# Optimization experiments

Measured on AMD Instinct MI355X. Metric: run time of the kernel, lower is better.

The kernel has to match this reference:

```python
import jax, jax.numpy as jnp
import numpy as np

N, F, E, B, D = 100000, 256, 128, 10000, 32
GAMMA, ZETA = -0.1, 1.1  # hard-concrete stretch params of L0Dense


def setup_inputs() -> dict:
    key = jax.random.key(0)
    ks = jax.random.split(key, 12)
    return {
        "nodes": jax.random.randint(ks[0], (B,), 0, N),
        "neigh_idx": jax.random.randint(ks[1], (B, D), 0, N),
        "neigh_mask": jax.random.bernoulli(ks[2], 0.9, (B, D)),
        "feature": jax.random.normal(ks[3], (N, F), jnp.float32),
        "W": jax.random.normal(ks[4], (F, E), jnp.float32) * 0.05,
        "b": jnp.zeros((E,), jnp.float32),
        "qz_loga": jax.random.normal(ks[5], (F,), jnp.float32),
        "att1_w": jax.random.normal(ks[6], (2 * E, E), jnp.float32) * 0.05,
        "att1_b": jnp.zeros((E,), jnp.float32),
        "att2_w": jax.random.normal(ks[7], (E, E), jnp.float32) * 0.05,
        "att2_b": jnp.zeros((E,), jnp.float32),
        "att3_w": jax.random.normal(ks[8], (E, 1), jnp.float32) * 0.05,
        "att3_b": jnp.zeros((1,), jnp.float32),
    }


def reference(nodes, neigh_idx, neigh_mask, feature, W, b, qz_loga,
              att1_w, att1_b, att2_w, att2_b, att3_w, att3_b):
    # L0Dense, deterministic (eval) hard-concrete gate on input dims
    z = jnp.clip(jax.nn.sigmoid(qz_loga) * (ZETA - GAMMA) + GAMMA, 0.0, 1.0)
    We = W * z[:, None]                                  # [F, E]

    node_feat = feature[nodes] @ We + b                   # [B, E]
    neigh_feat = feature[neigh_idx] @ We + b              # [B, D, E]

    # GraphRec-style attention MLP over (neighbor, center) pairs
    h = jnp.concatenate(
        [neigh_feat, jnp.broadcast_to(node_feat[:, None, :], neigh_feat.shape)],
        axis=-1)                                          # [B, D, 2E]
    h = jax.nn.relu(h @ att1_w + att1_b)
    h = jax.nn.relu(h @ att2_w + att2_b)
    scores = (h @ att3_w + att3_b)[..., 0]                # [B, D]
    scores = jnp.where(neigh_mask, scores, -1e30)
    att = jax.nn.softmax(scores, axis=-1)                 # [B, D]

    agg = jnp.einsum('bd,bde->be', att, neigh_feat)       # weighted sum
    has_neigh = neigh_mask.any(axis=-1, keepdims=True)
    return jnp.where(has_neigh, agg, node_feat)           # n==0 fallback
```

## Files before the change

kernel.cpp:

```cpp
#include <hip/hip_runtime.h>
#include <hip/hip_bf16.h>
#include <math.h>

#define NN 100000
#define FF 256
#define EE 128
#define BB_ 10000
#define DD 32

typedef __attribute__((ext_vector_type(8))) short short8;
typedef __attribute__((ext_vector_type(4))) float f32x4;

__device__ __forceinline__ short f2bf(float f) {
  __hip_bfloat16 h = __float2bfloat16(f);
  union { __hip_bfloat16 h; short s; } u; u.h = h;
  return u.s;
}
__device__ __forceinline__ float bf2f(short s) {
  union { unsigned u; float f; } v;
  v.u = ((unsigned)(unsigned short)s) << 16;
  return v.f;
}

__global__ __launch_bounds__(256) void k_prep(
    const float* __restrict__ W, const float* __restrict__ qz,
    const float* __restrict__ a1w, const float* __restrict__ a2w,
    const float* __restrict__ bb,
    float* __restrict__ Wef32, short* __restrict__ BT2,
    short* __restrict__ a1wTc, short* __restrict__ w2T,
    float* __restrict__ bias2) {
  int i = blockIdx.x * 256 + threadIdx.x;
  if (i < 32768) {
    int f = i >> 7, e = i & 127;
    float g = qz[f];
    float s = 1.0f / (1.0f + expf(-g));
    float z = fminf(fmaxf(s * 1.2f - 0.1f, 0.0f), 1.0f);
    float v = W[f * 128 + e] * z;
    Wef32[f * 128 + e] = v;
    BT2[e * 256 + f] = f2bf(v);
  } else if (i < 49152) {
    int t = i - 32768; int n = t >> 7, k = t & 127;
    a1wTc[n * 128 + k] = f2bf(a1w[(128 + k) * 128 + n]);
  } else if (i < 65536) {
    int t = i - 49152; int n = t >> 7, k = t & 127;
    w2T[n * 128 + k] = f2bf(a2w[k * 128 + n]);
  } else if (i < 65664) {
    bias2[i - 65536] = bb[i - 65536];
  }
}

__global__ __launch_bounds__(256) void k_compose(
    const float* __restrict__ Wef32, const float* __restrict__ a1w,
    const float* __restrict__ a1b, const float* __restrict__ bb,
    short* __restrict__ BT2, float* __restrict__ bias2) {
  const int n = blockIdx.x;
  const int f = threadIdx.x;
  float s = 0.f;
  for (int e = 0; e < 128; ++e)
    s = fmaf(a1w[e * 128 + n], Wef32[f * 128 + e], s);
  BT2[(size_t)(128 + n) * 256 + f] = f2bf(s);
  if (f == 0) {
    float by = a1b[n];
    for (int e = 0; e < 128; ++e) by = fmaf(bb[e], a1w[e * 128 + n], by);
    bias2[128 + n] = by;
  }
}

template <int K, int LDA, int LDC, bool AF32, bool OUTBF16>
__global__ __launch_bounds__(256) void k_mm(
    const void* __restrict__ Ap, const short* __restrict__ BT,
    const float* __restrict__ bias, const int* __restrict__ idx,
    void* __restrict__ Cp, int M) {
  __shared__ short As[128 * 64];
  __shared__ short Bs[128 * 64];
  const int tid = threadIdx.x;
  const int mb = blockIdx.x * 128;
  const int col0 = blockIdx.y * 128;
  const int wave = tid >> 6, lane = tid & 63;
  const int wr = wave >> 1, wc = wave & 1;
  const int l15 = lane & 15, lg = lane >> 4;

  size_t abase[4];
#pragma unroll
  for (int s = 0; s < 4; ++s) {
    int row = (tid + s * 256) >> 3;
    int grow = mb + row;
    int gr = 0;
    if (grow < M) gr = idx ? idx[grow] : grow;
    abase[s] = (size_t)gr * LDA;
  }

  f32x4 acc[4][4];
#pragma unroll
  for (int i = 0; i < 4; ++i)
#pragma unroll
    for (int j = 0; j < 4; ++j) acc[i][j] = (f32x4){0.f, 0.f, 0.f, 0.f};

  for (int k0 = 0; k0 < K; k0 += 64) {
#pragma unroll
    for (int s = 0; s < 4; ++s) {
      int q = tid + s * 256;
      int row = q >> 3, c = q & 7;
      short8 av;
      if (AF32) {
        const float* ap = (const float*)Ap + abase[s] + k0 + c * 8;
        float4 f0 = *(const float4*)ap;
        float4 f1 = *(const float4*)(ap + 4);
        av[0] = f2bf(f0.x); av[1] = f2bf(f0.y);
        av[2] = f2bf(f0.z); av[3] = f2bf(f0.w);
        av[4] = f2bf(f1.x); av[5] = f2bf(f1.y);
        av[6] = f2bf(f1.z); av[7] = f2bf(f1.w);
      } else {
        av = *(const short8*)((const short*)Ap + abase[s] + k0 + c * 8);
      }
      *(short8*)(As + row * 64 + 8 * (c ^ (row & 7))) = av;
      short8 bv = *(const short8*)(BT + (size_t)(col0 + row) * K + k0 + c * 8);
      *(short8*)(Bs + row * 64 + 8 * (c ^ (row & 7))) = bv;
    }
    __syncthreads();
#pragma unroll
    for (int ks = 0; ks < 2; ++ks) {
      int c = ks * 4 + lg;
      short8 af[4], bfv[4];
#pragma unroll
      for (int i = 0; i < 4; ++i) {
        int r = wr * 64 + i * 16 + l15;
        af[i] = *(short8*)(As + r * 64 + 8 * (c ^ (r & 7)));
        int n = wc * 64 + i * 16 + l15;
        bfv[i] = *(short8*)(Bs + n * 64 + 8 * (c ^ (n & 7)));
      }
#pragma unroll
      for (int i = 0; i < 4; ++i)
#pragma unroll
        for (int j = 0; j < 4; ++j)
          acc[i][j] = __builtin_amdgcn_mfma_f32_16x16x32_bf16(
              af[i], bfv[j], acc[i][j], 0, 0, 0);
    }
    __syncthreads();
  }

  float bv4[4];
#pragma unroll
  for (int j = 0; j < 4; ++j) {
    int col = wc * 64 + j * 16 + l15;
    bv4[j] = bias ? bias[col0 + col] : 0.f;
  }
#pragma unroll
  for (int i = 0; i < 4; ++i) {
#pragma unroll
    for (int r = 0; r < 4; ++r) {
      int row = mb + wr * 64 + i * 16 + lg * 4 + r;
      if (row < M) {
#pragma unroll
        for (int j = 0; j < 4; ++j) {
          int col = wc * 64 + j * 16 + l15;
          float v = acc[i][j][r] + bv4[j];
          if (OUTBF16)
            ((short*)Cp)[(size_t)row * LDC + col0 + col] = f2bf(v);
          else
            ((float*)Cp)[(size_t)row * LDC + col0 + col] = v;
        }
      }
    }
  }
}

__global__ __launch_bounds__(256) void k_attn4(
    const short* __restrict__ XY, const float* __restrict__ P,
    const int* __restrict__ nodes, const int* __restrict__ nidx,
    const int* __restrict__ nmask, const short* __restrict__ w2T,
    const float* __restrict__ b2, const float* __restrict__ w3,
    const float* __restrict__ b3, float* __restrict__ out) {
  __shared__ int ni_s[4][32];
  __shared__ float sc_s[4][32];
  __shared__ float att_s[4][32];
  const int tid = threadIdx.x;
  const int wave = tid >> 6, lane = tid & 63;
  const int b = blockIdx.x * 4 + wave;
  const int l15 = lane & 15, lg = lane >> 4;

  if (lane < 32) ni_s[wave][lane] = nidx[b * DD + lane];

  const int m = nmask[(size_t)b * DD + (lane & 31)];
  const int nid0 = ni_s[wave][l15];
  const int nid1 = ni_s[wave][16 + l15];
  const short* yr0 = XY + (size_t)nid0 * 256 + 128;
  const short* yr1 = XY + (size_t)nid1 * 256 + 128;
  short8 y0v[4], y1v[4];
#pragma unroll
  for (int ks = 0; ks < 4; ++ks) {
    const int k0 = ks * 32 + lg * 8;
    y0v[ks] = *(const short8*)(yr0 + k0);
    y1v[ks] = *(const short8*)(yr1 + k0);
  }
  unsigned xv[32];
#pragma unroll
  for (int d = 0; d < 32; ++d)
    xv[d] = *(const unsigned*)(XY + (size_t)ni_s[wave][d] * 256 + 2 * lane);

  const float* pr = P + (size_t)b * EE;

  f32x4 acc[2][8];
#pragma unroll
  for (int i = 0; i < 2; ++i)
#pragma unroll
    for (int j = 0; j < 8; ++j) acc[i][j] = (f32x4){0.f, 0.f, 0.f, 0.f};

#pragma unroll
  for (int ks = 0; ks < 4; ++ks) {
    const int k0 = ks * 32 + lg * 8;
    float4 pa = *(const float4*)(pr + k0);
    float4 pb = *(const float4*)(pr + k0 + 4);
    float pf[8] = {pa.x, pa.y, pa.z, pa.w, pb.x, pb.y, pb.z, pb.w};
    short8 a0, a1;
#pragma unroll
    for (int e = 0; e < 8; ++e) {
      a0[e] = f2bf(fmaxf(bf2f(y0v[ks][e]) + pf[e], 0.f));
      a1[e] = f2bf(fmaxf(bf2f(y1v[ks][e]) + pf[e], 0.f));
    }
    short8 bfv[8];
#pragma unroll
    for (int j = 0; j < 8; ++j)
      bfv[j] = *(const short8*)(w2T + (size_t)(j * 16 + l15) * EE + k0);
    __builtin_amdgcn_s_setprio(1);
#pragma unroll
    for (int j = 0; j < 8; ++j) {
      acc[0][j] = __builtin_amdgcn_mfma_f32_16x16x32_bf16(a0, bfv[j],
                                                          acc[0][j], 0, 0, 0);
      acc[1][j] = __builtin_amdgcn_mfma_f32_16x16x32_bf16(a1, bfv[j],
                                                          acc[1][j], 0, 0, 0);
    }
    __builtin_amdgcn_s_setprio(0);
  }

  float b2v[8], w3v[8];
#pragma unroll
  for (int j = 0; j < 8; ++j) {
    int col = j * 16 + l15;
    b2v[j] = b2[col];
    w3v[j] = w3[col];
  }
  float part[2][4];
#pragma unroll
  for (int i = 0; i < 2; ++i)
#pragma unroll
    for (int r = 0; r < 4; ++r) {
      float s = 0.f;
#pragma unroll
      for (int j = 0; j < 8; ++j)
        s += fmaxf(acc[i][j][r] + b2v[j], 0.f) * w3v[j];
      part[i][r] = s;
    }
#pragma unroll
  for (int off = 1; off <= 8; off <<= 1) {
#pragma unroll
    for (int i = 0; i < 2; ++i)
#pragma unroll
      for (int r = 0; r < 4; ++r) part[i][r] += __shfl_xor(part[i][r], off);
  }
  if (l15 == 0) {
#pragma unroll
    for (int i = 0; i < 2; ++i)
#pragma unroll
      for (int r = 0; r < 4; ++r)
        sc_s[wave][i * 16 + lg * 4 + r] = part[i][r];
  }

  const int row = lane & 31;
  float s = sc_s[wave][row] + b3[0];
  if (!m) s = -1e30f;
  float mx = s;
#pragma unroll
  for (int off = 1; off <= 16; off <<= 1) mx = fmaxf(mx, __shfl_xor(mx, off));
  float e = expf(s - mx);
  float sum = e;
#pragma unroll
  for (int off = 1; off <= 16; off <<= 1) sum += __shfl_xor(sum, off);
  if (lane < 32) att_s[wave][row] = e / sum;
  const bool has = (__ballot(m != 0) != 0ull);

  float a0 = 0.f, a1 = 0.f;
  if (has) {
#pragma unroll
    for (int d = 0; d < 32; ++d) {
      float a = att_s[wave][d];
      a0 += a * bf2f((short)(xv[d] & 0xffffu));
      a1 += a * bf2f((short)(xv[d] >> 16));
    }
  } else {
    const short* xr = XY + (size_t)nodes[b] * 256;
    unsigned x2 = *(const unsigned*)(xr + 2 * lane);
    a0 = bf2f((short)(x2 & 0xffffu));
    a1 = bf2f((short)(x2 >> 16));
  }
  *(float2*)(out + (size_t)b * EE + 2 * lane) = make_float2(a0, a1);
}

extern "C" void kernel_launch(void* const* d_in, const int* in_sizes, int n_in,
                              void* d_out, int out_size, void* d_ws,
                              size_t ws_size, hipStream_t stream) {
  const int* nodes = (const int*)d_in[0];
  const int* nidx = (const int*)d_in[1];
  const int* nmask = (const int*)d_in[2];
  const float* feature = (const float*)d_in[3];
  const float* W = (const float*)d_in[4];
  const float* bb = (const float*)d_in[5];
  const float* qz = (const float*)d_in[6];
  const float* a1w = (const float*)d_in[7];
  const float* a1b = (const float*)d_in[8];
  const float* a2w = (const float*)d_in[9];
  const float* a2b = (const float*)d_in[10];
  const float* a3w = (const float*)d_in[11];
  const float* a3b = (const float*)d_in[12];
  float* out = (float*)d_out;

  char* ws = (char*)d_ws;
  short* BT2   = (short*)(ws);
  float* Wef32 = (float*)(ws + 131072);
  short* a1wTc = (short*)(ws + 262144);
  short* w2T   = (short*)(ws + 294912);
  float* bias2 = (float*)(ws + 327680);
  short* XYb   = (short*)(ws + 524288);
  float* Pv    = (float*)(ws + 524288 + 51200000);

  k_prep<<<257, 256, 0, stream>>>(W, qz, a1w, a2w, bb, Wef32, BT2, a1wTc, w2T,
                                  bias2);
  k_compose<<<128, 256, 0, stream>>>(Wef32, a1w, a1b, bb, BT2, bias2);
  k_mm<256, 256, 256, true, true><<<dim3((NN + 127) / 128, 2), 256, 0,
                                    stream>>>(feature, BT2, bias2, nullptr,
                                              XYb, NN);
  k_mm<128, 256, 128, false, false><<<dim3((BB_ + 127) / 128, 1), 256, 0,
                                      stream>>>(XYb, a1wTc, nullptr, nodes, Pv,
                                                BB_);
  k_attn4<<<BB_ / 4, 256, 0, stream>>>(XYb, Pv, nodes, nidx, nmask, w2T, a2b,
                                       a3w, a3b, out);
}
```

Before: 137.2 us.

## Replace generic feature GEMM with single-pass full-width XY projection kernel

```diff
diff --git a/kernel.cpp b/kernel.cpp
--- a/kernel.cpp
+++ b/kernel.cpp
@@ -66,6 +66,82 @@
   }
 }
 
+__global__ __launch_bounds__(512) void k_xy(
+    const float* __restrict__ feat, const short* __restrict__ BT2,
+    const float* __restrict__ bias2, short* __restrict__ XY, int M) {
+  __shared__ short As[128 * 256];
+  const int tid = threadIdx.x;
+  const int mb = blockIdx.x * 128;
+  const int wave = tid >> 6, lane = tid & 63;
+  const int wr = wave >> 2, wn = wave & 3;
+  const int l15 = lane & 15, lg = lane >> 4;
+
+#pragma unroll
+  for (int s = 0; s < 8; ++s) {
+    int q = tid + s * 512;
+    int row = q >> 5, c = q & 31;
+    int grow = mb + row;
+    if (grow >= M) grow = M - 1;
+    const float* ap = feat + (size_t)grow * 256 + c * 8;
+    float4 f0 = *(const float4*)ap;
+    float4 f1 = *(const float4*)(ap + 4);
+    short8 av;
+    av[0] = f2bf(f0.x); av[1] = f2bf(f0.y);
+    av[2] = f2bf(f0.z); av[3] = f2bf(f0.w);
+    av[4] = f2bf(f1.x); av[5] = f2bf(f1.y);
+    av[6] = f2bf(f1.z); av[7] = f2bf(f1.w);
+    *(short8*)(As + row * 256 + 8 * (c ^ (row & 7))) = av;
+  }
+  __syncthreads();
+
+  f32x4 acc[4][4];
+#pragma unroll
+  for (int i = 0; i < 4; ++i)
+#pragma unroll
+    for (int j = 0; j < 4; ++j) acc[i][j] = (f32x4){0.f, 0.f, 0.f, 0.f};
+
+  const short* bbase = BT2 + (size_t)(wn * 64 + l15) * 256;
+#pragma unroll
+  for (int ks = 0; ks < 8; ++ks) {
+    const int cc = ks * 4 + lg;
+    short8 af[4], bf4[4];
+#pragma unroll
+    for (int i = 0; i < 4; ++i) {
+      int r = wr * 64 + i * 16 + l15;
+      af[i] = *(short8*)(As + r * 256 + 8 * (cc ^ (r & 7)));
+    }
+#pragma unroll
+    for (int j = 0; j < 4; ++j)
+      bf4[j] = *(const short8*)(bbase + j * 16 * 256 + cc * 8);
+    __builtin_amdgcn_s_setprio(1);
+#pragma unroll
+    for (int i = 0; i < 4; ++i)
+#pragma unroll
+      for (int j = 0; j < 4; ++j)
+        acc[i][j] = __builtin_amdgcn_mfma_f32_16x16x32_bf16(
+            af[i], bf4[j], acc[i][j], 0, 0, 0);
+    __builtin_amdgcn_s_setprio(0);
+  }
+
+  float bv4[4];
+#pragma unroll
+  for (int j = 0; j < 4; ++j) bv4[j] = bias2[wn * 64 + j * 16 + l15];
+#pragma unroll
+  for (int i = 0; i < 4; ++i) {
+#pragma unroll
+    for (int r = 0; r < 4; ++r) {
+      int row = mb + wr * 64 + i * 16 + lg * 4 + r;
+      if (row < M) {
+#pragma unroll
+        for (int j = 0; j < 4; ++j) {
+          int col = wn * 64 + j * 16 + l15;
+          XY[(size_t)row * 256 + col] = f2bf(acc[i][j][r] + bv4[j]);
+        }
+      }
+    }
+  }
+}
+
 template <int K, int LDA, int LDC, bool AF32, bool OUTBF16>
 __global__ __launch_bounds__(256) void k_mm(
     const void* __restrict__ Ap, const short* __restrict__ BT,
@@ -326,9 +402,7 @@
   k_prep<<<257, 256, 0, stream>>>(W, qz, a1w, a2w, bb, Wef32, BT2, a1wTc, w2T,
                                   bias2);
   k_compose<<<128, 256, 0, stream>>>(Wef32, a1w, a1b, bb, BT2, bias2);
-  k_mm<256, 256, 256, true, true><<<dim3((NN + 127) / 128, 2), 256, 0,
-                                    stream>>>(feature, BT2, bias2, nullptr,
-                                              XYb, NN);
+  k_xy<<<(NN + 127) / 128, 512, 0, stream>>>(feature, BT2, bias2, XYb, NN);
   k_mm<128, 256, 128, false, false><<<dim3((BB_ + 127) / 128, 1), 256, 0,
                                       stream>>>(XYb, a1wTc, nullptr, nodes, Pv,
                                                 BB_);
```

Measured after the change: 139.5 us. No clear change (+1.7%).
